# Kernel tuning notes

Measured on AMD Instinct MI355X. Metric: run time of the kernel, lower is better.

The kernel has to match this reference:

```python
import jax, jax.numpy as jnp
import numpy as np

N = 100000       # nodes
E = 1600000      # edges
IN = 256         # in_channels
H = 64           # hidden_channels
OUT = 40         # out_channels
K = 3            # hops

def setup_inputs() -> dict:
    key = jax.random.key(0)
    ks = jax.random.split(key, 20)
    f = lambda k, s: jax.random.normal(k, s, dtype=jnp.float32) * 0.05
    return {
        'x': f(ks[0], (N, IN)),
        'edge_index': jax.random.randint(ks[1], (2, E), 0, N),
        'W_in': f(ks[2], (H, IN)), 'b_in': f(ks[3], (H,)),
        'sg_W': f(ks[4], (K, H, H)), 'sg_b': f(ks[5], (K, H)),
        'in_proj_W': f(ks[6], (3 * H, H)), 'in_proj_b': f(ks[7], (3 * H,)),
        'out_W': f(ks[8], (H, H)), 'out_b': f(ks[9], (H,)),
        'ff_W1': f(ks[10], (2 * H, H)), 'ff_b1': f(ks[11], (2 * H,)),
        'ff_W2': f(ks[12], (H, 2 * H)), 'ff_b2': f(ks[13], (H,)),
        'ln1_w': jnp.ones((H,), jnp.float32), 'ln1_b': jnp.zeros((H,), jnp.float32),
        'ln2_w': jnp.ones((H,), jnp.float32), 'ln2_b': jnp.zeros((H,), jnp.float32),
        'cls_W': f(ks[14], (OUT, H)), 'cls_b': f(ks[15], (OUT,)),
    }

def _ln(x, w, b, eps=1e-5):
    m = x.mean(-1, keepdims=True)
    v = ((x - m) ** 2).mean(-1, keepdims=True)
    return (x - m) * jax.lax.rsqrt(v + eps) * w + b

def reference(x, edge_index, W_in, b_in, sg_W, sg_b, in_proj_W, in_proj_b,
              out_W, out_b, ff_W1, ff_b1, ff_W2, ff_b2,
              ln1_w, ln1_b, ln2_w, ln2_b, cls_W, cls_b):
    # --- gcn_norm with self loops (SGConv default) ---
    loop = jnp.arange(N)
    src = jnp.concatenate([edge_index[0], loop])
    dst = jnp.concatenate([edge_index[1], loop])
    deg = jax.ops.segment_sum(jnp.ones(src.shape[0], x.dtype), dst, num_segments=N)
    dinv = jnp.where(deg > 0, jax.lax.rsqrt(deg), 0.0)
    norm = dinv[src] * dinv[dst]  # [E+N]

    def prop(h):  # one symmetric-normalized propagation: S @ h
        return jax.ops.segment_sum(h[src] * norm[:, None], dst, num_segments=N)

    h0 = jax.nn.relu(x @ W_in.T + b_in)  # [N, H]
    # SGConv with K=hop recomputes S^hop h0; equivalently propagate iteratively
    tokens = [h0]
    p = h0
    for k in range(K):
        p = prop(p)
        tokens.append(jax.nn.relu(p @ sg_W[k].T + sg_b[k]))
    seq = jnp.stack(tokens, axis=1)  # [N, K+1, H]

    # --- TransformerEncoderLayer (nhead=1, post-norm, gelu), eval mode ---
    qkv = seq @ in_proj_W.T + in_proj_b
    q, kk, v = jnp.split(qkv, 3, axis=-1)
    scores = jnp.einsum('nsh,nth->nst', q, kk) / jnp.sqrt(jnp.asarray(H, seq.dtype))
    a = jnp.einsum('nst,nth->nsh', jax.nn.softmax(scores, axis=-1), v)
    a = a @ out_W.T + out_b
    seq = _ln(seq + a, ln1_w, ln1_b)
    ff = jax.nn.gelu(seq @ ff_W1.T + ff_b1, approximate=False) @ ff_W2.T + ff_b2
    seq = _ln(seq + ff, ln2_w, ln2_b)

    h = seq.mean(axis=1)  # [N, H]
    return h @ cls_W.T + cls_b  # [N, OUT]
```

## Files before the change

### kernel.cpp

```cpp
#include <hip/hip_runtime.h>
#include <hip/hip_bf16.h>
#include <math.h>

#define NN 100000
#define EE 1600000
#define OUTC 40
#define NB 391
#define NG 6250
#define CAP 64
#define NBIN 391
#define BCAP 6144

#define WP_WIN 0
#define WP_SG  16896
#define WP_QKV 30720
#define WP_WO  44544
#define WP_W1  49152
#define WP_W2  58368
#define WP_WC  67072
#define WP_TOT 70528

typedef __hip_bfloat16 bf16;
typedef __attribute__((ext_vector_type(8))) short bf16x8;
typedef __attribute__((ext_vector_type(4))) float f32x4;

__device__ __forceinline__ unsigned short f2us(float f){
  bf16 b = __float2bfloat16(f);
  unsigned short u; __builtin_memcpy(&u, &b, 2); return u;
}
__device__ __forceinline__ float us2f(unsigned short u){
  union{unsigned x; float f;} c; c.x = ((unsigned)u)<<16; return c.f;
}
__device__ __forceinline__ float lo_f(unsigned u){ union{unsigned x;float f;}c; c.x = u<<16; return c.f; }
__device__ __forceinline__ float hi_f(unsigned u){ union{unsigned x;float f;}c; c.x = u & 0xffff0000u; return c.f; }

__device__ __forceinline__ float gelu_f(float v){
  float ax = fabsf(v);
  float t  = __builtin_amdgcn_rcpf(fmaf(0.3275911f, ax, 1.0f));
  float p  = fmaf(t, 1.061405429f, -1.453152027f);
  p = fmaf(t, p, 1.421413741f);
  p = fmaf(t, p, -0.284496736f);
  p = fmaf(t, p, 0.254829592f);
  p = p * t;
  float ex = __expf(-ax*ax);
  float er = fmaf(-p, ex, 1.0f);
  er = copysignf(er, v);
  return 0.5f * v * (1.0f + er);
}

__global__ void k_wprep(const float* __restrict__ Win, const float* __restrict__ sgW,
                        const float* __restrict__ Wqkv, const float* __restrict__ Wo,
                        const float* __restrict__ W1, const float* __restrict__ W2,
                        const float* __restrict__ Wc, unsigned short* __restrict__ wp){
  for (int idx = blockIdx.x*blockDim.x + threadIdx.x; idx < WP_TOT;
       idx += gridDim.x*blockDim.x){
    float v; int o;
    if (idx < WP_SG){ o = idx; int r=o/264, c=o-r*264; v = (c<256)? Win[r*256+c] : 0.f; }
    else if (idx < WP_QKV){ o = idx-WP_SG; int h=o/4608, rem=o-h*4608, r=rem/72, c=rem-r*72;
      v=(c<64)? sgW[h*4096+r*64+c] : 0.f; }
    else if (idx < WP_WO){ o = idx-WP_QKV; int r=o/72, c=o-r*72; v=(c<64)? Wqkv[r*64+c]:0.f; }
    else if (idx < WP_W1){ o = idx-WP_WO; int r=o/72, c=o-r*72; v=(c<64)? Wo[r*64+c]:0.f; }
    else if (idx < WP_W2){ o = idx-WP_W1; int r=o/72, c=o-r*72; v=(c<64)? W1[r*64+c]:0.f; }
    else if (idx < WP_WC){ o = idx-WP_W2; int r=o/136, c=o-r*136; v=(c<128)? W2[r*128+c]:0.f; }
    else { o = idx-WP_WC; int r=o/72, c=o-r*72; v=(r<OUTC && c<64)? Wc[r*64+c]:0.f; }
    wp[idx] = f2us(v);
  }
}

__global__ void k_zero(int* p, int n){
  int i = blockIdx.x*blockDim.x + threadIdx.x;
  if (i < n) p[i] = 0;
}

__global__ void __launch_bounds__(256) k_bin(const int* __restrict__ ei,
    int* __restrict__ binFill, int2* __restrict__ binned){
  __shared__ int hist[NBIN], sbase[NBIN], loc[NBIN];
  const int tid = threadIdx.x;
  const int CH = (EE + gridDim.x - 1) / gridDim.x;
  const int e0 = blockIdx.x * CH;
  const int e1 = min(e0 + CH, EE);
  for (int i = tid; i < NBIN; i += 256){ hist[i] = 0; loc[i] = 0; }
  __syncthreads();
  for (int e = e0 + tid; e < e1; e += 256)
    atomicAdd(&hist[ei[EE + e] >> 8], 1);
  __syncthreads();
  for (int i = tid; i < NBIN; i += 256)
    sbase[i] = atomicAdd(&binFill[i], hist[i]);
  __syncthreads();
  for (int e = e0 + tid; e < e1; e += 256){
    int d = ei[EE + e];
    int s = ei[e];
    int b = d >> 8;
    int p = sbase[b] + atomicAdd(&loc[b], 1);
    if (p < BCAP) binned[(size_t)b*BCAP + p] = make_int2(s, d);
  }
}
__global__ void __launch_bounds__(256) k_bucket(const int* __restrict__ binFill,
    const int2* __restrict__ binned, int* __restrict__ srcb,
    int* __restrict__ cnt, float* __restrict__ dinv){
  __shared__ int lcnt[256];
  const int b = blockIdx.x, tid = threadIdx.x;
  lcnt[tid] = 0;
  __syncthreads();
  int m = binFill[b]; if (m > BCAP) m = BCAP;
  const int2* seg = binned + (size_t)b*BCAP;
  for (int e = tid; e < m; e += 256){
    int2 sd = seg[e];
    int dl = sd.y & 255;
    int p = atomicAdd(&lcnt[dl], 1);
    if (p < CAP) srcb[((size_t)(b << 8) + dl)*CAP + p] = sd.x;
  }
  __syncthreads();
  int d = (b << 8) + tid;
  if (d < NN){
    int c = lcnt[tid];
    dinv[d] = rsqrtf((float)c + 1.0f);
    cnt[d] = min(c, CAP);
  }
}

#define GACC(r, wt) \
  a0 += lo_f((r).x)*(wt); a1 += hi_f((r).x)*(wt); \
  a2 += lo_f((r).y)*(wt); a3 += hi_f((r).y)*(wt); \
  a4 += lo_f((r).z)*(wt); a5 += hi_f((r).z)*(wt); \
  a6 += lo_f((r).w)*(wt); a7 += hi_f((r).w)*(wt);

__global__ void __launch_bounds__(256) k_gather(const int* __restrict__ cnt,
    const int* __restrict__ srcb, const float* __restrict__ dinv,
    const unsigned short* __restrict__ prev, unsigned short* __restrict__ cur){
  int wid = (blockIdx.x*256 + threadIdx.x) >> 6;
  if (wid >= NN) return;
  const int lane = threadIdx.x & 63;
  const int grp = lane >> 3, cl = lane & 7;
  const int n = wid;
  const int deg = cnt[n];
  const int* bk = srcb + (size_t)n*CAP;
  const float dn = dinv[n];
  uint4 sr = *(const uint4*)(prev + ((size_t)n << 6) + (cl << 3));
  int sv[8];
  #pragma unroll
  for (int j = 0; j < 8; ++j){
    sv[j] = n;
    if (j*8 < deg){
      int idx = j*8 + grp;
      if (idx < deg) sv[j] = bk[idx];
    }
  }
  float wv[8];
  #pragma unroll
  for (int j = 0; j < 8; ++j){
    wv[j] = 0.f;
    if (j*8 < deg){
      int idx = j*8 + grp;
      if (idx < deg) wv[j] = dinv[sv[j]] * dn;
    }
  }
  uint4 rr[8];
  #pragma unroll
  for (int j = 0; j < 8; ++j){
    if (j*8 < deg)
      rr[j] = *(const uint4*)(prev + ((size_t)sv[j] << 6) + (cl << 3));
  }
  float a0=0,a1=0,a2=0,a3=0,a4=0,a5=0,a6=0,a7=0;
  #pragma unroll
  for (int j = 0; j < 8; ++j){
    if (j*8 < deg){ GACC(rr[j], wv[j]); }
  }
  a0 += __shfl_xor(a0,8); a0 += __shfl_xor(a0,16); a0 += __shfl_xor(a0,32);
  a1 += __shfl_xor(a1,8); a1 += __shfl_xor(a1,16); a1 += __shfl_xor(a1,32);
  a2 += __shfl_xor(a2,8); a2 += __shfl_xor(a2,16); a2 += __shfl_xor(a2,32);
  a3 += __shfl_xor(a3,8); a3 += __shfl_xor(a3,16); a3 += __shfl_xor(a3,32);
  a4 += __shfl_xor(a4,8); a4 += __shfl_xor(a4,16); a4 += __shfl_xor(a4,32);
  a5 += __shfl_xor(a5,8); a5 += __shfl_xor(a5,16); a5 += __shfl_xor(a5,32);
  a6 += __shfl_xor(a6,8); a6 += __shfl_xor(a6,16); a6 += __shfl_xor(a6,32);
  a7 += __shfl_xor(a7,8); a7 += __shfl_xor(a7,16); a7 += __shfl_xor(a7,32);
  if (lane < 8){
    float d2 = dn*dn;
    GACC(sr, d2);
    uint4 pk;
    pk.x = (unsigned)f2us(a0) | ((unsigned)f2us(a1) << 16);
    pk.y = (unsigned)f2us(a2) | ((unsigned)f2us(a3) << 16);
    pk.z = (unsigned)f2us(a4) | ((unsigned)f2us(a5) << 16);
    pk.w = (unsigned)f2us(a6) | ((unsigned)f2us(a7) << 16);
    *(uint4*)(cur + ((size_t)n << 6) + (cl << 3)) = pk;
  }
}

__global__ void __launch_bounds__(256) k_h0(const float* __restrict__ x,
    const unsigned short* __restrict__ wp, const float* __restrict__ bin,
    unsigned short* __restrict__ tokB, unsigned short* __restrict__ p0){
  __shared__ __align__(16) unsigned short Xs[64*264];
  __shared__ __align__(16) unsigned short Ws[64*264];
  __shared__ float bs[64];
  const int tid = threadIdx.x;
  {
    const uint4* src = (const uint4*)(wp + WP_WIN);
    for (int idx = tid; idx < 2112; idx += 256) ((uint4*)Ws)[idx] = src[idx];
  }
  const int n0 = blockIdx.x * 64;
  for (int idx = tid; idx < 4096; idx += 256){
    int r = idx >> 6, c0 = (idx & 63) * 4;
    int n = n0 + r; if (n >= NN) n = NN-1;
    float4 v = *(const float4*)(x + (size_t)n*256 + c0);
    unsigned short* d = &Xs[r*264 + c0];
    d[0]=f2us(v.x); d[1]=f2us(v.y); d[2]=f2us(v.z); d[3]=f2us(v.w);
  }
  if (tid < 64) bs[tid] = bin[tid];
  __syncthreads();
  const int w = tid >> 6, lane = tid & 63, quad = lane >> 4, c = lane & 15;
  f32x4 acc[4] = {{0,0,0,0},{0,0,0,0},{0,0,0,0},{0,0,0,0}};
  #pragma unroll
  for (int ks = 0; ks < 8; ++ks){
    int k0 = ks*32 + quad*8;
    bf16x8 a = *(const bf16x8*)&Xs[(w*16 + c)*264 + k0];
    #pragma unroll
    for (int nt = 0; nt < 4; ++nt){
      bf16x8 b = *(const bf16x8*)&Ws[(nt*16 + c)*264 + k0];
      acc[nt] = __builtin_amdgcn_mfma_f32_16x16x32_bf16(a, b, acc[nt], 0,0,0);
    }
  }
  __syncthreads();
  #pragma unroll
  for (int nt = 0; nt < 4; ++nt){
    int col = nt*16 + c;
    float bb = bs[col];
    #pragma unroll
    for (int rg = 0; rg < 4; ++rg){
      int rloc = w*16 + quad*4 + rg;
      Xs[rloc*72 + col] = f2us(fmaxf(acc[nt][rg] + bb, 0.f));
    }
  }
  __syncthreads();
  for (int idx = tid; idx < 512; idx += 256){
    int r = idx >> 3, ch = idx & 7;
    int n = n0 + r;
    if (n < NN){
      uint4 v = *(const uint4*)&Xs[r*72 + ch*8];
      *(uint4*)(tokB + (size_t)n*64 + ch*8) = v;
      *(uint4*)(p0   + (size_t)n*64 + ch*8) = v;
    }
  }
}

__global__ void __launch_bounds__(256) k_token(const unsigned short* __restrict__ cur,
    const unsigned short* __restrict__ wsg, const float* __restrict__ sgb,
    unsigned short* __restrict__ tok){
  __shared__ __align__(16) unsigned short Xs[64*72];
  __shared__ __align__(16) unsigned short Ws[64*72];
  __shared__ float bs[64];
  const int tid = threadIdx.x;
  {
    const uint4* src = (const uint4*)wsg;
    for (int idx = tid; idx < 576; idx += 256) ((uint4*)Ws)[idx] = src[idx];
  }
  if (tid < 64) bs[tid] = sgb[tid];
  const int n0 = blockIdx.x*64;
  for (int idx = tid; idx < 512; idx += 256){
    int r = idx >> 3, ch = idx & 7;
    int n = n0 + r; if (n >= NN) n = NN-1;
    *(uint4*)&Xs[r*72 + ch*8] = *(const uint4*)(cur + (size_t)n*64 + ch*8);
  }
  __syncthreads();
  const int w = tid >> 6, lane = tid & 63, quad = lane >> 4, c = lane & 15;
  f32x4 acc[4] = {{0,0,0,0},{0,0,0,0},{0,0,0,0},{0,0,0,0}};
  #pragma unroll
  for (int ks = 0; ks < 2; ++ks){
    int k0 = ks*32 + quad*8;
    bf16x8 a = *(const bf16x8*)&Xs[(w*16 + c)*72 + k0];
    #pragma unroll
    for (int nt = 0; nt < 4; ++nt){
      bf16x8 b = *(const bf16x8*)&Ws[(nt*16 + c)*72 + k0];
      acc[nt] = __builtin_amdgcn_mfma_f32_16x16x32_bf16(a, b, acc[nt], 0,0,0);
    }
  }
  __syncthreads();
  #pragma unroll
  for (int nt = 0; nt < 4; ++nt){
    int col = nt*16 + c;
    float bb = bs[col];
    #pragma unroll
    for (int rg = 0; rg < 4; ++rg){
      int rloc = w*16 + quad*4 + rg;
      Xs[rloc*72 + col] = f2us(fmaxf(acc[nt][rg] + bb, 0.f));
    }
  }
  __syncthreads();
  for (int idx = tid; idx < 512; idx += 256){
    int r = idx >> 3, ch = idx & 7;
    int n = n0 + r;
    if (n < NN)
      *(uint4*)(tok + (size_t)n*64 + ch*8) = *(const uint4*)&Xs[r*72 + ch*8];
  }
}

__global__ void __launch_bounds__(256) k_attn(unsigned short* __restrict__ tokB,
    const unsigned short* __restrict__ wp, const float* __restrict__ bqkv,
    const float* __restrict__ bo, const float* __restrict__ ln1w,
    const float* __restrict__ ln1b){
  __shared__ __align__(16) unsigned short Xs[64*72];
  __shared__ float bq[192], bos[64], l1w[64], l1b[64];
  const int tid = threadIdx.x;
  if (tid < 192) bq[tid] = bqkv[tid];
  if (tid < 64){ bos[tid]=bo[tid]; l1w[tid]=ln1w[tid]; l1b[tid]=ln1b[tid]; }
  const int w = tid >> 6, lane = tid & 63, quad = lane >> 4, c = lane & 15;
  const int rw = w*16;
  const unsigned short* Wq  = wp + WP_QKV;
  const unsigned short* Wos = wp + WP_WO;
  for (int g = blockIdx.x; g < NG; g += gridDim.x){
    __syncthreads();
    for (int idx = tid; idx < 512; idx += 256){
      int r = idx >> 3, ch = idx & 7;
      int t = r & 3, n = g*16 + (r >> 2);
      *(uint4*)&Xs[r*72 + ch*8] = *(const uint4*)(tokB + ((size_t)t*NN + n)*64 + ch*8);
    }
    __syncthreads();
    bf16x8 a0 = *(const bf16x8*)&Xs[(rw+c)*72 + quad*8];
    bf16x8 a1 = *(const bf16x8*)&Xs[(rw+c)*72 + 32 + quad*8];
    float resv[4][4];
    #pragma unroll
    for (int nt = 0; nt < 4; ++nt){
      #pragma unroll
      for (int rg = 0; rg < 4; ++rg)
        resv[nt][rg] = us2f(Xs[(rw + quad*4 + rg)*72 + nt*16 + c]);
    }
    f32x4 qk[12];
    #pragma unroll
    for (int nt = 0; nt < 12; ++nt){
      f32x4 acc = {0,0,0,0};
      bf16x8 b0 = *(const bf16x8*)&Wq[(nt*16+c)*72 + quad*8];
      bf16x8 b1 = *(const bf16x8*)&Wq[(nt*16+c)*72 + 32 + quad*8];
      acc = __builtin_amdgcn_mfma_f32_16x16x32_bf16(a0, b0, acc, 0,0,0);
      acc = __builtin_amdgcn_mfma_f32_16x16x32_bf16(a1, b1, acc, 0,0,0);
      float bb = bq[nt*16 + c];
      acc[0]+=bb; acc[1]+=bb; acc[2]+=bb; acc[3]+=bb;
      qk[nt] = acc;
    }
    float sc[4][4];
    #pragma unroll
    for (int s = 0; s < 4; ++s){
      #pragma unroll
      for (int t = 0; t < 4; ++t){
        float p = qk[0][s]*qk[4][t] + qk[1][s]*qk[5][t]
                + qk[2][s]*qk[6][t] + qk[3][s]*qk[7][t];
        p += __shfl_xor(p, 1); p += __shfl_xor(p, 2);
        p += __shfl_xor(p, 4); p += __shfl_xor(p, 8);
        sc[s][t] = p * 0.125f;
      }
    }
    float pm[4][4];
    #pragma unroll
    for (int s = 0; s < 4; ++s){
      float m = fmaxf(fmaxf(sc[s][0],sc[s][1]), fmaxf(sc[s][2],sc[s][3]));
      float e0=__expf(sc[s][0]-m), e1=__expf(sc[s][1]-m);
      float e2=__expf(sc[s][2]-m), e3=__expf(sc[s][3]-m);
      float inv = 1.f/(e0+e1+e2+e3);
      pm[s][0]=e0*inv; pm[s][1]=e1*inv; pm[s][2]=e2*inv; pm[s][3]=e3*inv;
    }
    #pragma unroll
    for (int tile = 0; tile < 4; ++tile){
      #pragma unroll
      for (int s = 0; s < 4; ++s){
        float av = pm[s][0]*qk[8+tile][0] + pm[s][1]*qk[8+tile][1]
                 + pm[s][2]*qk[8+tile][2] + pm[s][3]*qk[8+tile][3];
        Xs[(rw + quad*4 + s)*72 + tile*16 + c] = f2us(av);
      }
    }
    bf16x8 p0 = *(const bf16x8*)&Xs[(rw+c)*72 + quad*8];
    bf16x8 p1 = *(const bf16x8*)&Xs[(rw+c)*72 + 32 + quad*8];
    f32x4 ov[4];
    #pragma unroll
    for (int nt = 0; nt < 4; ++nt){
      f32x4 acc = {0,0,0,0};
      bf16x8 b0 = *(const bf16x8*)&Wos[(nt*16+c)*72 + quad*8];
      bf16x8 b1 = *(const bf16x8*)&Wos[(nt*16+c)*72 + 32 + quad*8];
      acc = __builtin_amdgcn_mfma_f32_16x16x32_bf16(p0, b0, acc, 0,0,0);
      acc = __builtin_amdgcn_mfma_f32_16x16x32_bf16(p1, b1, acc, 0,0,0);
      ov[nt] = acc;
    }
    float r4[4][4];
    #pragma unroll
    for (int nt = 0; nt < 4; ++nt){
      int col = nt*16 + c;
      float bb = bos[col];
      #pragma unroll
      for (int rg = 0; rg < 4; ++rg)
        r4[nt][rg] = ov[nt][rg] + bb + resv[nt][rg];
    }
    #pragma unroll
    for (int rg = 0; rg < 4; ++rg){
      float sm = r4[0][rg]+r4[1][rg]+r4[2][rg]+r4[3][rg];
      sm += __shfl_xor(sm,1); sm += __shfl_xor(sm,2);
      sm += __shfl_xor(sm,4); sm += __shfl_xor(sm,8);
      float mean = sm * (1.f/64.f);
      float d0=r4[0][rg]-mean, d1=r4[1][rg]-mean, d2=r4[2][rg]-mean, d3=r4[3][rg]-mean;
      float vs = d0*d0+d1*d1+d2*d2+d3*d3;
      vs += __shfl_xor(vs,1); vs += __shfl_xor(vs,2);
      vs += __shfl_xor(vs,4); vs += __shfl_xor(vs,8);
      float rinv = rsqrtf(vs*(1.f/64.f) + 1e-5f);
      int row = rw + quad*4 + rg;
      #pragma unroll
      for (int nt = 0; nt < 4; ++nt){
        int col = nt*16 + c;
        Xs[row*72 + col] = f2us((r4[nt][rg] - mean) * rinv * l1w[col] + l1b[col]);
      }
    }
    __syncthreads();
    for (int idx = tid; idx < 512; idx += 256){
      int r = idx >> 3, ch = idx & 7;
      int t = r & 3, n = g*16 + (r >> 2);
      *(uint4*)(tokB + ((size_t)t*NN + n)*64 + ch*8) = *(const uint4*)&Xs[r*72 + ch*8];
    }
  }
}

__global__ void __launch_bounds__(256) k_ffn(const unsigned short* __restrict__ tokB,
    const unsigned short* __restrict__ wp,
    const float* __restrict__ b1, const float* __restrict__ b2,
    const float* __restrict__ ln2w, const float* __restrict__ ln2b,
    const float* __restrict__ bc, float* __restrict__ out){
  __shared__ __align__(16) unsigned short Xs[64*72];
  __shared__ __align__(16) unsigned short F1[64*136];
  __shared__ __align__(16) unsigned short hsH[16*72];
  __shared__ __align__(16) unsigned short hsL[16*72];
  __shared__ float b1s[128], b2s[64], l2w[64], l2b[64], bcs[40];
  const int tid = threadIdx.x;
  if (tid < 128) b1s[tid] = b1[tid];
  if (tid < 64){ b2s[tid]=b2[tid]; l2w[tid]=ln2w[tid]; l2b[tid]=ln2b[tid]; }
  if (tid < 40)  bcs[tid] = bc[tid];
  const int w = tid >> 6, lane = tid & 63, quad = lane >> 4, c = lane & 15;
  const int rw = w*16;
  const unsigned short* W1g = wp + WP_W1;
  const unsigned short* W2g = wp + WP_W2;
  const unsigned short* Wcg = wp + WP_WC;
  for (int g = blockIdx.x; g < NG; g += gridDim.x){
    __syncthreads();
    for (int idx = tid; idx < 512; idx += 256){
      int r = idx >> 3, ch = idx & 7;
      int t = r & 3, n = g*16 + (r >> 2);
      *(uint4*)&Xs[r*72 + ch*8] = *(const uint4*)(tokB + ((size_t)t*NN + n)*64 + ch*8);
    }
    __syncthreads();
    bf16x8 a0 = *(const bf16x8*)&Xs[(rw+c)*72 + quad*8];
    bf16x8 a1 = *(const bf16x8*)&Xs[(rw+c)*72 + 32 + quad*8];
    #pragma unroll
    for (int nt = 0; nt < 8; ++nt){
      f32x4 acc = {0,0,0,0};
      bf16x8 b0 = *(const bf16x8*)&W1g[(nt*16+c)*72 + quad*8];
      bf16x8 b1v = *(const bf16x8*)&W1g[(nt*16+c)*72 + 32 + quad*8];
      acc = __builtin_amdgcn_mfma_f32_16x16x32_bf16(a0, b0, acc, 0,0,0);
      acc = __builtin_amdgcn_mfma_f32_16x16x32_bf16(a1, b1v, acc, 0,0,0);
      float bb = b1s[nt*16 + c];
      #pragma unroll
      for (int rg = 0; rg < 4; ++rg){
        float v = acc[rg] + bb;
        F1[(rw + quad*4 + rg)*136 + nt*16 + c] = f2us(gelu_f(v));
      }
    }
    bf16x8 fa[4];
    #pragma unroll
    for (int ks = 0; ks < 4; ++ks)
      fa[ks] = *(const bf16x8*)&F1[(rw+c)*136 + ks*32 + quad*8];
    f32x4 ov[4];
    #pragma unroll
    for (int nt = 0; nt < 4; ++nt){
      f32x4 acc = {0,0,0,0};
      #pragma unroll
      for (int ks = 0; ks < 4; ++ks){
        bf16x8 b = *(const bf16x8*)&W2g[(nt*16+c)*136 + ks*32 + quad*8];
        acc = __builtin_amdgcn_mfma_f32_16x16x32_bf16(fa[ks], b, acc, 0,0,0);
      }
      ov[nt] = acc;
    }
    float r4[4][4];
    #pragma unroll
    for (int nt = 0; nt < 4; ++nt){
      int col = nt*16 + c;
      float bb = b2s[col];
      #pragma unroll
      for (int rg = 0; rg < 4; ++rg){
        float seqv = us2f(Xs[(rw + quad*4 + rg)*72 + col]);
        r4[nt][rg] = ov[nt][rg] + bb + seqv;
      }
    }
    float hval[4] = {0.f, 0.f, 0.f, 0.f};
    #pragma unroll
    for (int rg = 0; rg < 4; ++rg){
      float sm = r4[0][rg]+r4[1][rg]+r4[2][rg]+r4[3][rg];
      sm += __shfl_xor(sm,1); sm += __shfl_xor(sm,2);
      sm += __shfl_xor(sm,4); sm += __shfl_xor(sm,8);
      float mean = sm * (1.f/64.f);
      float d0=r4[0][rg]-mean, d1=r4[1][rg]-mean, d2=r4[2][rg]-mean, d3=r4[3][rg]-mean;
      float vs = d0*d0+d1*d1+d2*d2+d3*d3;
      vs += __shfl_xor(vs,1); vs += __shfl_xor(vs,2);
      vs += __shfl_xor(vs,4); vs += __shfl_xor(vs,8);
      float rinv = rsqrtf(vs*(1.f/64.f) + 1e-5f);
      #pragma unroll
      for (int nt = 0; nt < 4; ++nt){
        int col = nt*16 + c;
        hval[nt] += (r4[nt][rg] - mean) * rinv * l2w[col] + l2b[col];
      }
    }
    #pragma unroll
    for (int nt = 0; nt < 4; ++nt){
      float hv = hval[nt] * 0.25f;
      unsigned short hh = f2us(hv);
      float lo = hv - us2f(hh);
      hsH[(w*4 + quad)*72 + nt*16 + c] = hh;
      hsL[(w*4 + quad)*72 + nt*16 + c] = f2us(lo);
    }
    __syncthreads();
    if (w < 3){
      bf16x8 hA0 = *(const bf16x8*)&hsH[c*72 + quad*8];
      bf16x8 hA1 = *(const bf16x8*)&hsH[c*72 + 32 + quad*8];
      bf16x8 lA0 = *(const bf16x8*)&hsL[c*72 + quad*8];
      bf16x8 lA1 = *(const bf16x8*)&hsL[c*72 + 32 + quad*8];
      bf16x8 wB0 = *(const bf16x8*)&Wcg[(w*16 + c)*72 + quad*8];
      bf16x8 wB1 = *(const bf16x8*)&Wcg[(w*16 + c)*72 + 32 + quad*8];
      f32x4 acc = {0,0,0,0};
      acc = __builtin_amdgcn_mfma_f32_16x16x32_bf16(hA0, wB0, acc, 0,0,0);
      acc = __builtin_amdgcn_mfma_f32_16x16x32_bf16(hA1, wB1, acc, 0,0,0);
      acc = __builtin_amdgcn_mfma_f32_16x16x32_bf16(lA0, wB0, acc, 0,0,0);
      acc = __builtin_amdgcn_mfma_f32_16x16x32_bf16(lA1, wB1, acc, 0,0,0);
      int o = w*16 + c;
      if (o < OUTC){
        float bb = bcs[o];
        #pragma unroll
        for (int rg = 0; rg < 4; ++rg)
          out[(size_t)(g*16 + quad*4 + rg)*OUTC + o] = acc[rg] + bb;
      }
    }
  }
}

extern "C" void kernel_launch(void* const* d_in, const int* in_sizes, int n_in,
                              void* d_out, int out_size, void* d_ws, size_t ws_size,
                              hipStream_t stream) {
  const float* x    = (const float*)d_in[0];
  const int*   ei   = (const int*  )d_in[1];
  const float* Win  = (const float*)d_in[2];
  const float* bin  = (const float*)d_in[3];
  const float* sgW  = (const float*)d_in[4];
  const float* sgb  = (const float*)d_in[5];
  const float* Wqkv = (const float*)d_in[6];
  const float* bqkv = (const float*)d_in[7];
  const float* Wo   = (const float*)d_in[8];
  const float* bo   = (const float*)d_in[9];
  const float* W1   = (const float*)d_in[10];
  const float* b1   = (const float*)d_in[11];
  const float* W2   = (const float*)d_in[12];
  const float* b2   = (const float*)d_in[13];
  const float* ln1w = (const float*)d_in[14];
  const float* ln1b = (const float*)d_in[15];
  const float* ln2w = (const float*)d_in[16];
  const float* ln2b = (const float*)d_in[17];
  const float* Wc   = (const float*)d_in[18];
  const float* bc   = (const float*)d_in[19];

  char* ws = (char*)d_ws;
  float*          dinv = (float*)(ws);
  int*            cnt  = (int*  )(ws + 400128);
  unsigned short* wp   = (unsigned short*)(ws + 800256);
  unsigned short* tokB = (unsigned short*)(ws + 941568);
  unsigned short* pb0  = (unsigned short*)(ws + 52141696);
  unsigned short* pb1  = (unsigned short*)(ws + 64941824);
  int2* binned  = (int2*)pb0;
  int*  binFill = (int*)tokB;
  int*  srcb    = (int*)(tokB + (size_t)2*NN*64);

  k_wprep<<<128, 256, 0, stream>>>(Win, sgW, Wqkv, Wo, W1, W2, Wc, wp);

  k_zero  <<<2, 256, 0, stream>>>(binFill, NBIN);
  k_bin   <<<512, 256, 0, stream>>>(ei, binFill, binned);
  k_bucket<<<NBIN, 256, 0, stream>>>(binFill, binned, srcb, cnt, dinv);

  const int GB = (NN + 63) / 64;
  const int GG = (NN*64 + 255) / 256;
  k_h0<<<GB, 256, 0, stream>>>(x, wp, bin, tokB, pb0);

  k_gather<<<GG, 256, 0, stream>>>(cnt, srcb, dinv, pb0, pb1);
  k_token <<<GB, 256, 0, stream>>>(pb1, wp + WP_SG,        sgb,       tokB + (size_t)1*NN*64);
  k_gather<<<GG, 256, 0, stream>>>(cnt, srcb, dinv, pb1, pb0);
  k_gather<<<GG, 256, 0, stream>>>(cnt, srcb, dinv, pb0, pb1);
  k_token <<<GB, 256, 0, stream>>>(pb0, wp + WP_SG + 4608, sgb + 64,  tokB + (size_t)2*NN*64);
  k_token <<<GB, 256, 0, stream>>>(pb1, wp + WP_SG + 9216, sgb + 128, tokB + (size_t)3*NN*64);

  k_attn<<<2048, 256, 0, stream>>>(tokB, wp, bqkv, bo, ln1w, ln1b);
  k_ffn <<<2048, 256, 0, stream>>>(tokB, wp, b1, b2, ln2w, ln2b, bc, (float*)d_out);
}
```

Measured before the change: 617.3 us.

## Merge independent graph stages into shared launches and pack binned edges

Independent kernels are merged into single launches that branch on block index: binFill zeroing goes into weight prep, bucket into h0, token-1 into the second gather, and tokens 2 and 3 into one launch. The goal is fewer launches and idle tails between them. Binned edges are packed as a single int (24-bit source plus local destination), which halves the intermediate traffic. Attention keeps V in shared memory instead of registers and sets a launch bound of 5 blocks per SM to cut register pressure, at the cost of extra LDS traffic and merged kernels that take on the larger shared-memory footprint.

```diff
diff --git a/kernel.cpp b/kernel.cpp
--- a/kernel.cpp
+++ b/kernel.cpp
@@ -10,6 +10,8 @@
 #define CAP 64
 #define NBIN 391
 #define BCAP 6144
+#define GB 1563
+#define GG 25000
 
 #define WP_WIN 0
 #define WP_SG  16896
@@ -48,12 +50,18 @@
   return 0.5f * v * (1.0f + er);
 }
 
-__global__ void k_wprep(const float* __restrict__ Win, const float* __restrict__ sgW,
+__global__ void k_prep0(const float* __restrict__ Win, const float* __restrict__ sgW,
                         const float* __restrict__ Wqkv, const float* __restrict__ Wo,
                         const float* __restrict__ W1, const float* __restrict__ W2,
-                        const float* __restrict__ Wc, unsigned short* __restrict__ wp){
-  for (int idx = blockIdx.x*blockDim.x + threadIdx.x; idx < WP_TOT;
-       idx += gridDim.x*blockDim.x){
+                        const float* __restrict__ Wc, unsigned short* __restrict__ wp,
+                        int* __restrict__ binFill){
+  if (blockIdx.x < 2){
+    int i = blockIdx.x*256 + threadIdx.x;
+    if (i < NBIN) binFill[i] = 0;
+    return;
+  }
+  const int bid = blockIdx.x - 2;
+  for (int idx = bid*256 + threadIdx.x; idx < WP_TOT; idx += 128*256){
     float v; int o;
     if (idx < WP_SG){ o = idx; int r=o/264, c=o-r*264; v = (c<256)? Win[r*256+c] : 0.f; }
     else if (idx < WP_QKV){ o = idx-WP_SG; int h=o/4608, rem=o-h*4608, r=rem/72, c=rem-r*72;
@@ -67,13 +75,8 @@
   }
 }
 
-__global__ void k_zero(int* p, int n){
-  int i = blockIdx.x*blockDim.x + threadIdx.x;
-  if (i < n) p[i] = 0;
-}
-
 __global__ void __launch_bounds__(256) k_bin(const int* __restrict__ ei,
-    int* __restrict__ binFill, int2* __restrict__ binned){
+    int* __restrict__ binFill, int* __restrict__ binned){
   __shared__ int hist[NBIN], sbase[NBIN], loc[NBIN];
   const int tid = threadIdx.x;
   const int CH = (EE + gridDim.x - 1) / gridDim.x;
@@ -92,23 +95,24 @@
     int s = ei[e];
     int b = d >> 8;
     int p = sbase[b] + atomicAdd(&loc[b], 1);
-    if (p < BCAP) binned[(size_t)b*BCAP + p] = make_int2(s, d);
-  }
-}
-__global__ void __launch_bounds__(256) k_bucket(const int* __restrict__ binFill,
-    const int2* __restrict__ binned, int* __restrict__ srcb,
-    int* __restrict__ cnt, float* __restrict__ dinv){
-  __shared__ int lcnt[256];
-  const int b = blockIdx.x, tid = threadIdx.x;
+    if (p < BCAP) binned[(size_t)b*BCAP + p] = s | ((d & 255) << 24);
+  }
+}
+
+__device__ __forceinline__ void bucket_body(const int* __restrict__ binFill,
+    const int* __restrict__ binned, int* __restrict__ srcb,
+    int* __restrict__ cnt, float* __restrict__ dinv, int* lcnt, int b){
+  const int tid = threadIdx.x;
   lcnt[tid] = 0;
   __syncthreads();
   int m = binFill[b]; if (m > BCAP) m = BCAP;
-  const int2* seg = binned + (size_t)b*BCAP;
+  const int* seg = binned + (size_t)b*BCAP;
   for (int e = tid; e < m; e += 256){
-    int2 sd = seg[e];
-    int dl = sd.y & 255;
+    int v = seg[e];
+    int dl = ((unsigned)v) >> 24;
+    int s = v & 0xFFFFFF;
     int p = atomicAdd(&lcnt[dl], 1);
-    if (p < CAP) srcb[((size_t)(b << 8) + dl)*CAP + p] = sd.x;
+    if (p < CAP) srcb[((size_t)(b << 8) + dl)*CAP + p] = s;
   }
   __syncthreads();
   int d = (b << 8) + tid;
@@ -119,16 +123,87 @@
   }
 }
 
+__device__ __forceinline__ void h0_body(const float* __restrict__ x,
+    const unsigned short* __restrict__ wp, const float* __restrict__ bin,
+    unsigned short* __restrict__ tok0, unsigned short* __restrict__ p0,
+    unsigned short* Xs, unsigned short* Ws, float* bs, int bid){
+  const int tid = threadIdx.x;
+  {
+    const uint4* src = (const uint4*)(wp + WP_WIN);
+    for (int idx = tid; idx < 2112; idx += 256) ((uint4*)Ws)[idx] = src[idx];
+  }
+  const int n0 = bid * 64;
+  for (int idx = tid; idx < 4096; idx += 256){
+    int r = idx >> 6, c0 = (idx & 63) * 4;
+    int n = n0 + r; if (n >= NN) n = NN-1;
+    float4 v = *(const float4*)(x + (size_t)n*256 + c0);
+    unsigned short* d = &Xs[r*264 + c0];
+    d[0]=f2us(v.x); d[1]=f2us(v.y); d[2]=f2us(v.z); d[3]=f2us(v.w);
+  }
+  if (tid < 64) bs[tid] = bin[tid];
+  __syncthreads();
+  const int w = tid >> 6, lane = tid & 63, quad = lane >> 4, c = lane & 15;
+  f32x4 acc[4] = {{0,0,0,0},{0,0,0,0},{0,0,0,0},{0,0,0,0}};
+  #pragma unroll
+  for (int ks = 0; ks < 8; ++ks){
+    int k0 = ks*32 + quad*8;
+    bf16x8 a = *(const bf16x8*)&Xs[(w*16 + c)*264 + k0];
+    #pragma unroll
+    for (int nt = 0; nt < 4; ++nt){
+      bf16x8 b = *(const bf16x8*)&Ws[(nt*16 + c)*264 + k0];
+      acc[nt] = __builtin_amdgcn_mfma_f32_16x16x32_bf16(a, b, acc[nt], 0,0,0);
+    }
+  }
+  __syncthreads();
+  #pragma unroll
+  for (int nt = 0; nt < 4; ++nt){
+    int col = nt*16 + c;
+    float bb = bs[col];
+    #pragma unroll
+    for (int rg = 0; rg < 4; ++rg){
+      int rloc = w*16 + quad*4 + rg;
+      Xs[rloc*72 + col] = f2us(fmaxf(acc[nt][rg] + bb, 0.f));
+    }
+  }
+  __syncthreads();
+  for (int idx = tid; idx < 512; idx += 256){
+    int r = idx >> 3, ch = idx & 7;
+    int n = n0 + r;
+    if (n < NN){
+      uint4 v = *(const uint4*)&Xs[r*72 + ch*8];
+      *(uint4*)(tok0 + (size_t)n*64 + ch*8) = v;
+      *(uint4*)(p0   + (size_t)n*64 + ch*8) = v;
+    }
+  }
+}
+
+__global__ void __launch_bounds__(256) k_buckh0(const int* __restrict__ binFill,
+    const int* __restrict__ binned, int* __restrict__ srcb,
+    int* __restrict__ cnt, float* __restrict__ dinv,
+    const float* __restrict__ x, const unsigned short* __restrict__ wp,
+    const float* __restrict__ bin, unsigned short* __restrict__ tok0,
+    unsigned short* __restrict__ p0){
+  __shared__ __align__(16) unsigned short Xs[64*264];
+  __shared__ __align__(16) unsigned short Ws[64*264];
+  __shared__ float bs[64];
+  __shared__ int lcnt[256];
+  if (blockIdx.x < NBIN)
+    bucket_body(binFill, binned, srcb, cnt, dinv, lcnt, blockIdx.x);
+  else
+    h0_body(x, wp, bin, tok0, p0, Xs, Ws, bs, blockIdx.x - NBIN);
+}
+
 #define GACC(r, wt) \
   a0 += lo_f((r).x)*(wt); a1 += hi_f((r).x)*(wt); \
   a2 += lo_f((r).y)*(wt); a3 += hi_f((r).y)*(wt); \
   a4 += lo_f((r).z)*(wt); a5 += hi_f((r).z)*(wt); \
   a6 += lo_f((r).w)*(wt); a7 += hi_f((r).w)*(wt);
 
-__global__ void __launch_bounds__(256) k_gather(const int* __restrict__ cnt,
+__device__ __forceinline__ void gather_body(const int* __restrict__ cnt,
     const int* __restrict__ srcb, const float* __restrict__ dinv,
-    const unsigned short* __restrict__ prev, unsigned short* __restrict__ cur){
-  int wid = (blockIdx.x*256 + threadIdx.x) >> 6;
+    const unsigned short* __restrict__ prev, unsigned short* __restrict__ cur,
+    int bid){
+  int wid = (bid << 2) + (threadIdx.x >> 6);
   if (wid >= NN) return;
   const int lane = threadIdx.x & 63;
   const int grp = lane >> 3, cl = lane & 7;
@@ -186,75 +261,23 @@
   }
 }
 
-__global__ void __launch_bounds__(256) k_h0(const float* __restrict__ x,
-    const unsigned short* __restrict__ wp, const float* __restrict__ bin,
-    unsigned short* __restrict__ tokB, unsigned short* __restrict__ p0){
-  __shared__ __align__(16) unsigned short Xs[64*264];
-  __shared__ __align__(16) unsigned short Ws[64*264];
-  __shared__ float bs[64];
-  const int tid = threadIdx.x;
-  {
-    const uint4* src = (const uint4*)(wp + WP_WIN);
-    for (int idx = tid; idx < 2112; idx += 256) ((uint4*)Ws)[idx] = src[idx];
-  }
-  const int n0 = blockIdx.x * 64;
-  for (int idx = tid; idx < 4096; idx += 256){
-    int r = idx >> 6, c0 = (idx & 63) * 4;
-    int n = n0 + r; if (n >= NN) n = NN-1;
-    float4 v = *(const float4*)(x + (size_t)n*256 + c0);
-    unsigned short* d = &Xs[r*264 + c0];
-    d[0]=f2us(v.x); d[1]=f2us(v.y); d[2]=f2us(v.z); d[3]=f2us(v.w);
-  }
-  if (tid < 64) bs[tid] = bin[tid];
-  __syncthreads();
-  const int w = tid >> 6, lane = tid & 63, quad = lane >> 4, c = lane & 15;
-  f32x4 acc[4] = {{0,0,0,0},{0,0,0,0},{0,0,0,0},{0,0,0,0}};
-  #pragma unroll
-  for (int ks = 0; ks < 8; ++ks){
-    int k0 = ks*32 + quad*8;
-    bf16x8 a = *(const bf16x8*)&Xs[(w*16 + c)*264 + k0];
-    #pragma unroll
-    for (int nt = 0; nt < 4; ++nt){
-      bf16x8 b = *(const bf16x8*)&Ws[(nt*16 + c)*264 + k0];
-      acc[nt] = __builtin_amdgcn_mfma_f32_16x16x32_bf16(a, b, acc[nt], 0,0,0);
-    }
-  }
-  __syncthreads();
-  #pragma unroll
-  for (int nt = 0; nt < 4; ++nt){
-    int col = nt*16 + c;
-    float bb = bs[col];
-    #pragma unroll
-    for (int rg = 0; rg < 4; ++rg){
-      int rloc = w*16 + quad*4 + rg;
-      Xs[rloc*72 + col] = f2us(fmaxf(acc[nt][rg] + bb, 0.f));
-    }
-  }
-  __syncthreads();
-  for (int idx = tid; idx < 512; idx += 256){
-    int r = idx >> 3, ch = idx & 7;
-    int n = n0 + r;
-    if (n < NN){
-      uint4 v = *(const uint4*)&Xs[r*72 + ch*8];
-      *(uint4*)(tokB + (size_t)n*64 + ch*8) = v;
-      *(uint4*)(p0   + (size_t)n*64 + ch*8) = v;
-    }
-  }
-}
-
-__global__ void __launch_bounds__(256) k_token(const unsigned short* __restrict__ cur,
+__global__ void __launch_bounds__(256) k_gather(const int* __restrict__ cnt,
+    const int* __restrict__ srcb, const float* __restrict__ dinv,
+    const unsigned short* __restrict__ prev, unsigned short* __restrict__ cur){
+  gather_body(cnt, srcb, dinv, prev, cur, blockIdx.x);
+}
+
+__device__ __forceinline__ void tok_body(const unsigned short* __restrict__ cur,
     const unsigned short* __restrict__ wsg, const float* __restrict__ sgb,
-    unsigned short* __restrict__ tok){
-  __shared__ __align__(16) unsigned short Xs[64*72];
-  __shared__ __align__(16) unsigned short Ws[64*72];
-  __shared__ float bs[64];
+    unsigned short* __restrict__ tok,
+    unsigned short* Xs, unsigned short* Ws, float* bs, int bid){
   const int tid = threadIdx.x;
   {
     const uint4* src = (const uint4*)wsg;
     for (int idx = tid; idx < 576; idx += 256) ((uint4*)Ws)[idx] = src[idx];
   }
   if (tid < 64) bs[tid] = sgb[tid];
-  const int n0 = blockIdx.x*64;
+  const int n0 = bid*64;
   for (int idx = tid; idx < 512; idx += 256){
     int r = idx >> 3, ch = idx & 7;
     int n = n0 + r; if (n >= NN) n = NN-1;
@@ -293,17 +316,48 @@
   }
 }
 
-__global__ void __launch_bounds__(256) k_attn(unsigned short* __restrict__ tokB,
+__global__ void __launch_bounds__(256) k_tokgather(
+    const unsigned short* __restrict__ tcur, const unsigned short* __restrict__ wsg,
+    const float* __restrict__ sgb, unsigned short* __restrict__ tok,
+    const int* __restrict__ cnt, const int* __restrict__ srcb,
+    const float* __restrict__ dinv, const unsigned short* __restrict__ prev,
+    unsigned short* __restrict__ cur){
+  __shared__ __align__(16) unsigned short Xs[64*72];
+  __shared__ __align__(16) unsigned short Ws[64*72];
+  __shared__ float bs[64];
+  if (blockIdx.x < GB)
+    tok_body(tcur, wsg, sgb, tok, Xs, Ws, bs, blockIdx.x);
+  else
+    gather_body(cnt, srcb, dinv, prev, cur, blockIdx.x - GB);
+}
+
+__global__ void __launch_bounds__(256) k_tok23(
+    const unsigned short* __restrict__ curA, const unsigned short* __restrict__ wsgA,
+    const float* __restrict__ sgbA, unsigned short* __restrict__ tokA,
+    const unsigned short* __restrict__ curB, const unsigned short* __restrict__ wsgB,
+    const float* __restrict__ sgbB, unsigned short* __restrict__ tokOutB){
+  __shared__ __align__(16) unsigned short Xs[64*72];
+  __shared__ __align__(16) unsigned short Ws[64*72];
+  __shared__ float bs[64];
+  if (blockIdx.x < GB)
+    tok_body(curA, wsgA, sgbA, tokA, Xs, Ws, bs, blockIdx.x);
+  else
+    tok_body(curB, wsgB, sgbB, tokOutB, Xs, Ws, bs, blockIdx.x - GB);
+}
+
+__global__ void __launch_bounds__(256, 5) k_attn(unsigned short* __restrict__ tokB,
     const unsigned short* __restrict__ wp, const float* __restrict__ bqkv,
     const float* __restrict__ bo, const float* __restrict__ ln1w,
     const float* __restrict__ ln1b){
   __shared__ __align__(16) unsigned short Xs[64*72];
+  __shared__ float Vs[16*272];
   __shared__ float bq[192], bos[64], l1w[64], l1b[64];
   const int tid = threadIdx.x;
   if (tid < 192) bq[tid] = bqkv[tid];
   if (tid < 64){ bos[tid]=bo[tid]; l1w[tid]=ln1w[tid]; l1b[tid]=ln1b[tid]; }
   const int w = tid >> 6, lane = tid & 63, quad = lane >> 4, c = lane & 15;
   const int rw = w*16;
+  const int vbase = (w*4 + quad)*272 + c;
   const unsigned short* Wq  = wp + WP_QKV;
   const unsigned short* Wos = wp + WP_WO;
   for (int g = blockIdx.x; g < NG; g += gridDim.x){
@@ -323,7 +377,7 @@
       for (int rg = 0; rg < 4; ++rg)
         resv[nt][rg] = us2f(Xs[(rw + quad*4 + rg)*72 + nt*16 + c]);
     }
-    f32x4 qk[12];
+    f32x4 qk[8];
     #pragma unroll
     for (int nt = 0; nt < 12; ++nt){
       f32x4 acc = {0,0,0,0};
@@ -333,7 +387,12 @@
       acc = __builtin_amdgcn_mfma_f32_16x16x32_bf16(a1, b1, acc, 0,0,0);
       float bb = bq[nt*16 + c];
       acc[0]+=bb; acc[1]+=bb; acc[2]+=bb; acc[3]+=bb;
-      qk[nt] = acc;
+      if (nt < 8) qk[nt] = acc;
+      else {
+        #pragma unroll
+        for (int t = 0; t < 4; ++t)
+          Vs[vbase + ((nt-8)*4 + t)*16] = acc[t];
+      }
     }
     float sc[4][4];
     #pragma unroll
@@ -358,10 +417,13 @@
     }
     #pragma unroll
     for (int tile = 0; tile < 4; ++tile){
+      float v0 = Vs[vbase + (tile*4+0)*16];
+      float v1 = Vs[vbase + (tile*4+1)*16];
+      float v2 = Vs[vbase + (tile*4+2)*16];
+      float v3 = Vs[vbase + (tile*4+3)*16];
       #pragma unroll
       for (int s = 0; s < 4; ++s){
-        float av = pm[s][0]*qk[8+tile][0] + pm[s][1]*qk[8+tile][1]
-                 + pm[s][2]*qk[8+tile][2] + pm[s][3]*qk[8+tile][3];
+        float av = pm[s][0]*v0 + pm[s][1]*v1 + pm[s][2]*v2 + pm[s][3]*v3;
         Xs[(rw + quad*4 + s)*72 + tile*16 + c] = f2us(av);
       }
     }
@@ -557,32 +619,26 @@
   const float* bc   = (const float*)d_in[19];
 
   char* ws = (char*)d_ws;
-  float*          dinv = (float*)(ws);
-  int*            cnt  = (int*  )(ws + 400128);
-  unsigned short* wp   = (unsigned short*)(ws + 800256);
-  unsigned short* tokB = (unsigned short*)(ws + 941568);
-  unsigned short* pb0  = (unsigned short*)(ws + 52141696);
-  unsigned short* pb1  = (unsigned short*)(ws + 64941824);
-  int2* binned  = (int2*)pb0;
-  int*  binFill = (int*)tokB;
-  int*  srcb    = (int*)(tokB + (size_t)2*NN*64);
-
-  k_wprep<<<128, 256, 0, stream>>>(Win, sgW, Wqkv, Wo, W1, W2, Wc, wp);
-
-  k_zero  <<<2, 256, 0, stream>>>(binFill, NBIN);
-  k_bin   <<<512, 256, 0, stream>>>(ei, binFill, binned);
-  k_bucket<<<NBIN, 256, 0, stream>>>(binFill, binned, srcb, cnt, dinv);
-
-  const int GB = (NN + 63) / 64;
-  const int GG = (NN*64 + 255) / 256;
-  k_h0<<<GB, 256, 0, stream>>>(x, wp, bin, tokB, pb0);
-
-  k_gather<<<GG, 256, 0, stream>>>(cnt, srcb, dinv, pb0, pb1);
-  k_token <<<GB, 256, 0, stream>>>(pb1, wp + WP_SG,        sgb,       tokB + (size_t)1*NN*64);
+  float*          dinv    = (float*)(ws);
+  int*            cnt     = (int*  )(ws + 400128);
+  unsigned short* wp      = (unsigned short*)(ws + 800256);
+  int*            binFill = (int*)(ws + 941312);
+  unsigned short* tokB    = (unsigned short*)(ws + 943104);
+  unsigned short* pb0     = (unsigned short*)(ws + 52143104);
+  unsigned short* pb1     = (unsigned short*)(ws + 64943104);
+  int* binned = (int*)(tokB + (size_t)1*NN*64);
+  int* srcb   = (int*)(tokB + (size_t)2*NN*64);
+
+  k_prep0<<<130, 256, 0, stream>>>(Win, sgW, Wqkv, Wo, W1, W2, Wc, wp, binFill);
+  k_bin<<<512, 256, 0, stream>>>(ei, binFill, binned);
+  k_buckh0<<<NBIN + GB, 256, 0, stream>>>(binFill, binned, srcb, cnt, dinv,
+                                          x, wp, bin, tokB, pb1);
   k_gather<<<GG, 256, 0, stream>>>(cnt, srcb, dinv, pb1, pb0);
-  k_gather<<<GG, 256, 0, stream>>>(cnt, srcb, dinv, pb0, pb1);
-  k_token <<<GB, 256, 0, stream>>>(pb0, wp + WP_SG + 4608, sgb + 64,  tokB + (size_t)2*NN*64);
-  k_token <<<GB, 256, 0, stream>>>(pb1, wp + WP_SG + 9216, sgb + 128, tokB + (size_t)3*NN*64);
+  k_tokgather<<<GB + GG, 256, 0, stream>>>(pb0, wp + WP_SG, sgb, tokB + (size_t)1*NN*64,
+                                           cnt, srcb, dinv, pb0, pb1);
+  k_gather<<<GG, 256, 0, stream>>>(cnt, srcb, dinv, pb1, pb0);
+  k_tok23<<<2*GB, 256, 0, stream>>>(pb1, wp + WP_SG + 4608, sgb + 64,  tokB + (size_t)2*NN*64,
+                                    pb0, wp + WP_SG + 9216, sgb + 128, tokB + (size_t)3*NN*64);
 
   k_attn<<<2048, 256, 0, stream>>>(tokB, wp, bqkv, bo, ln1w, ln1b);
   k_ffn <<<2048, 256, 0, stream>>>(tokB, wp, b1, b2, ln2w, ln2b, bc, (float*)d_out);
```

After: 710.0 us. +15.0%, slower.
